# Kernel optimization log

Hardware: AMD Instinct MI355X
Metric: run time of the kernel (lower is better)

The kernel has to match this reference:

```python
import jax, jax.numpy as jnp
import numpy as np

N, E, G = 20000, 320000, 64
DIN, H, EF, FC, OUT = 128, 256, 16, 256, 1
BN_EPS = 1e-5


def _gine_layer(x, src, dst, edge_attr, We, be, Wa, ba, g, bt, Wb, bb):
    # GINEConv (eps=0): out = mlp(x + sum_j relu(x_j + lin_edge(e_ij)))
    e = edge_attr @ We.T + be                      # [E, in_ch]
    m = jax.nn.relu(x[src] + e)                    # messages [E, in_ch]
    agg = jax.ops.segment_sum(m, dst, num_segments=x.shape[0])
    h = (x + agg) @ Wa.T + ba                      # Linear
    # BatchNorm1d in eval mode with running_mean=0, running_var=1
    inv = jax.lax.rsqrt(jnp.asarray(1.0 + BN_EPS, h.dtype))
    h = jax.nn.relu(h * inv * g + bt)
    return jax.nn.relu(h @ Wb.T + bb)


def _mean_pool(h, batch, num_graphs):
    sums = jax.ops.segment_sum(h, batch, num_segments=num_graphs)
    cnt = jax.ops.segment_sum(jnp.ones((h.shape[0],), h.dtype), batch, num_segments=num_graphs)
    return sums / jnp.maximum(cnt, 1.0)[:, None]


def setup_inputs() -> dict:
    key = jax.random.key(0)
    ks = iter(jax.random.split(key, 64))

    def nrm(shape, s=0.05):
        return jax.random.normal(next(ks), shape, jnp.float32) * s

    inp = {
        "x": jax.random.normal(next(ks), (N, DIN), jnp.float32),
        "edge_attr": jax.random.normal(next(ks), (E, EF), jnp.float32),
        "src": jax.random.randint(next(ks), (E,), 0, N),
        "dst": jax.random.randint(next(ks), (E,), 0, N),
        "batch": jnp.sort(jax.random.randint(next(ks), (N,), 0, G)),
    }
    dims = [(DIN, H), (H, H), (H, H)]
    for i, (din, h) in enumerate(dims, start=1):
        inp[f"We{i}"] = nrm((din, EF));  inp[f"be{i}"] = jnp.zeros((din,), jnp.float32)
        inp[f"Wa{i}"] = nrm((h, din));  inp[f"ba{i}"] = jnp.zeros((h,), jnp.float32)
        inp[f"g{i}"] = jnp.ones((h,), jnp.float32); inp[f"bt{i}"] = jnp.zeros((h,), jnp.float32)
        inp[f"Wb{i}"] = nrm((h, h));    inp[f"bb{i}"] = jnp.zeros((h,), jnp.float32)
    inp["L1w"] = nrm((FC * 3, H * 3)); inp["L1b"] = jnp.zeros((FC * 3,), jnp.float32)
    inp["L2w"] = nrm((OUT, FC * 3));   inp["L2b"] = jnp.zeros((OUT,), jnp.float32)
    return inp


def reference(x, edge_attr, src, dst, batch,
              We1, be1, Wa1, ba1, g1, bt1, Wb1, bb1,
              We2, be2, Wa2, ba2, g2, bt2, Wb2, bb2,
              We3, be3, Wa3, ba3, g3, bt3, Wb3, bb3,
              L1w, L1b, L2w, L2b):
    h1 = _gine_layer(x,  src, dst, edge_attr, We1, be1, Wa1, ba1, g1, bt1, Wb1, bb1)
    h2 = _gine_layer(h1, src, dst, edge_attr, We2, be2, Wa2, ba2, g2, bt2, Wb2, bb2)
    h3 = _gine_layer(h2, src, dst, edge_attr, We3, be3, Wa3, ba3, g3, bt3, Wb3, bb3)
    p = jnp.concatenate([_mean_pool(h1, batch, G),
                         _mean_pool(h2, batch, G),
                         _mean_pool(h3, batch, G)], axis=1)   # [G, 3H]
    h = jax.nn.relu(p @ L1w.T + L1b)   # dropout is identity (training=False)
    return jax.nn.sigmoid(h @ L2w.T + L2b)
```

## Files before the change

kernel.cpp:

```cpp
#include <hip/hip_runtime.h>
#include <math.h>
#include <stdint.h>

#define N_NODES 20000
#define M_PAD 20032
#define N_EDGES 320000
#define N_GRAPHS 64
#define DIN 128
#define H 256
#define POOL_W 768
#define CHUNK 40
#define NCHUNK (N_EDGES / CHUNK)

typedef __attribute__((ext_vector_type(8))) short bf16x8;
typedef __attribute__((ext_vector_type(4))) float f32x4;
typedef __attribute__((ext_vector_type(4))) unsigned int u32x4;
typedef __attribute__((ext_vector_type(2))) unsigned int u32x2;
typedef _Float16 h2 __attribute__((ext_vector_type(2)));

__device__ __forceinline__ unsigned short f2bf(float f) {
    unsigned u = __builtin_bit_cast(unsigned, f);
    u += 0x7FFFu + ((u >> 16) & 1u);
    return (unsigned short)(u >> 16);
}
__device__ __forceinline__ float bf2f(unsigned short u) {
    return __builtin_bit_cast(float, (unsigned)u << 16);
}
__device__ __forceinline__ unsigned short f2h(float f) {
    const _Float16 h = (_Float16)f;
    return __builtin_bit_cast(unsigned short, h);
}

#if __has_builtin(__builtin_amdgcn_fdot2)
#define DOT2(a, b, c) __builtin_amdgcn_fdot2((a), (b), (c), false)
#else
__device__ __forceinline__ float dot2_fallback(h2 a, h2 b, float c) {
    return fmaf((float)a.x, (float)b.x, fmaf((float)a.y, (float)b.y, c));
}
#define DOT2(a, b, c) dot2_fallback((a), (b), (c))
#endif

struct CvtJob  { const float* s; unsigned short* d; int n4; int mode; };
struct CvtJobs { CvtJob j[12]; };

__global__ __launch_bounds__(256) void cvt_all(CvtJobs jobs)
{
    const CvtJob J = jobs.j[blockIdx.y];
    if (J.mode == 2) {
        const ushort4 z = {0, 0, 0, 0};
        for (int i = blockIdx.x * 256 + threadIdx.x; i < J.n4; i += gridDim.x * 256)
            ((ushort4*)J.d)[i] = z;
        return;
    }
    if (J.mode == 1) {
        for (int i = blockIdx.x * 256 + threadIdx.x; i < J.n4; i += gridDim.x * 256) {
            const float4 v = ((const float4*)J.s)[i];
            ushort4 r;
            r.x = f2h(v.x); r.y = f2h(v.y); r.z = f2h(v.z); r.w = f2h(v.w);
            ((ushort4*)J.d)[i] = r;
        }
        return;
    }
    for (int i = blockIdx.x * 256 + threadIdx.x; i < J.n4; i += gridDim.x * 256) {
        const float4 v = ((const float4*)J.s)[i];
        ushort4 r;
        r.x = f2bf(v.x); r.y = f2bf(v.y); r.z = f2bf(v.z); r.w = f2bf(v.w);
        ((ushort4*)J.d)[i] = r;
    }
}

__global__ __launch_bounds__(256) void hist_kernel(const int* __restrict__ dst,
                                                   int* __restrict__ deg)
{
    const int i = blockIdx.x * 256 + threadIdx.x;
    if (i < N_EDGES) atomicAdd(deg + dst[i], 1);
}

__global__ __launch_bounds__(1024) void scan_kernel(const int* __restrict__ deg,
                                                    int* __restrict__ off,
                                                    int* __restrict__ cur,
                                                    const int* __restrict__ batch,
                                                    int* __restrict__ start)
{
    __shared__ int wsum[16];
    __shared__ int carry;
    const int tid = threadIdx.x, wave = tid >> 6, lane = tid & 63;
    if (tid == 0) carry = 0;
    __syncthreads();
    for (int base = 0; base < N_NODES; base += 1024) {
        const int i = base + tid;
        const int v = (i < N_NODES) ? deg[i] : 0;
        int s = v;
#pragma unroll
        for (int d = 1; d < 64; d <<= 1) {
            const int t = __shfl_up(s, d);
            if (lane >= d) s += t;
        }
        if (lane == 63) wsum[wave] = s;
        __syncthreads();
        if (wave == 0) {
            int t = (lane < 16) ? wsum[lane] : 0;
#pragma unroll
            for (int d = 1; d < 16; d <<= 1) {
                const int u = __shfl_up(t, d);
                if (lane >= d) t += u;
            }
            if (lane < 16) wsum[lane] = t;
        }
        __syncthreads();
        const int wbase = (wave == 0) ? 0 : wsum[wave - 1];
        if (i < N_NODES) {
            const int o = carry + wbase + s - v;
            off[i] = o;
            cur[i] = o;
        }
        const int tot = wsum[15];
        __syncthreads();
        if (tid == 0) carry += tot;
        __syncthreads();
    }
    if (tid == 0) off[N_NODES] = carry;

    if (tid <= N_GRAPHS) {
        if (tid == N_GRAPHS) { start[N_GRAPHS] = N_NODES; }
        else {
            int lo = 0, hi = N_NODES;
            while (lo < hi) { const int mid = (lo + hi) >> 1; if (batch[mid] < tid) lo = mid + 1; else hi = mid; }
            start[tid] = lo;
        }
    }
}

__global__ __launch_bounds__(256) void chunkmap_kernel(const int* __restrict__ off,
                                                       int* __restrict__ cmap)
{
    const int w = blockIdx.x * 256 + threadIdx.x;
    if (w > NCHUNK) return;
    if (w == NCHUNK) { cmap[w] = N_NODES; return; }
    const int target = w * CHUNK;
    int lo = 0, hi = N_NODES;
    while (lo < hi) { const int mid = (lo + hi) >> 1; if (off[mid] < target) lo = mid + 1; else hi = mid; }
    cmap[w] = lo;
}

__global__ __launch_bounds__(256) void scatter_kernel(
    const int* __restrict__ src, const int* __restrict__ dst,
    const float* __restrict__ ea, int* __restrict__ cursor,
    int* __restrict__ ssrc, unsigned short* __restrict__ eas)
{
    const int e = blockIdx.x * 256 + threadIdx.x;
    if (e < N_EDGES) {
        const int p = atomicAdd(cursor + dst[e], 1);
        ssrc[p] = src[e];
        const float4* er = (const float4*)(ea + (size_t)e * 16);
        unsigned short* dr = eas + (size_t)p * 16;
        ushort4* d4 = (ushort4*)dr;
#pragma unroll
        for (int q = 0; q < 4; ++q) {
            const float4 v = er[q];
            ushort4 r;
            r.x = f2h(v.x); r.y = f2h(v.y); r.z = f2h(v.z); r.w = f2h(v.w);
            d4[q] = r;
        }
    }
}

template<int IN>
__global__ __launch_bounds__(256) void agg3(
    const unsigned short* __restrict__ xb,
    const unsigned short* __restrict__ eas,
    const int* __restrict__ ssrc,
    const int* __restrict__ off,
    const int* __restrict__ cmap,
    const unsigned short* __restrict__ Weh,
    const float* __restrict__ be,
    unsigned short* __restrict__ out)
{
    constexpr int CPL = IN / 64;
    constexpr int XW  = CPL / 2;
    const int lane = threadIdx.x & 63;
    const int wid  = blockIdx.x * 4 + (threadIdx.x >> 6);
    const int c0 = lane * CPL;
    const int zd = __builtin_amdgcn_mbcnt_lo(0u, 0u);

    u32x4 wlo[CPL], whi[CPL];
    float bias[CPL], acc[CPL];
#pragma unroll
    for (int j = 0; j < CPL; ++j) {
        const u32x4* wr = (const u32x4*)(Weh + (size_t)(c0 + j) * 16);
        wlo[j] = wr[0];
        whi[j] = wr[1];
        bias[j] = be[c0 + j];
        acc[j]  = 0.0f;
    }
#pragma unroll
    for (int j = 0; j < CPL; ++j) {
#pragma unroll
        for (int k = 0; k < 4; ++k) {
            { float t = __builtin_bit_cast(float, wlo[j][k]); asm volatile("" : "+v"(t)); wlo[j][k] = __builtin_bit_cast(unsigned int, t); }
            { float t = __builtin_bit_cast(float, whi[j][k]); asm volatile("" : "+v"(t)); whi[j][k] = __builtin_bit_cast(unsigned int, t); }
        }
        asm volatile("" : "+v"(bias[j]));
    }

    int n          = __builtin_amdgcn_readfirstlane(cmap[wid]);
    const int nend = __builtin_amdgcn_readfirstlane(cmap[wid + 1]);
    if (n >= nend) return;
    int p          = __builtin_amdgcn_readfirstlane(off[n]);
    const int pend = __builtin_amdgcn_readfirstlane(off[nend]);

    auto flush = [&](int nn) {
        if constexpr (XW == 2) {
            const u32x2 xs = *(const u32x2*)(xb + (size_t)nn * IN + c0);
            const float x0 = __builtin_bit_cast(float, xs[0] << 16);
            const float x1 = __builtin_bit_cast(float, xs[0] & 0xFFFF0000u);
            const float x2 = __builtin_bit_cast(float, xs[1] << 16);
            const float x3 = __builtin_bit_cast(float, xs[1] & 0xFFFF0000u);
            u32x2 o;
            o[0] = (unsigned)f2bf(x0 + acc[0]) | ((unsigned)f2bf(x1 + acc[1]) << 16);
            o[1] = (unsigned)f2bf(x2 + acc[2]) | ((unsigned)f2bf(x3 + acc[3]) << 16);
            *(u32x2*)(out + (size_t)nn * IN + c0) = o;
        } else {
            const unsigned int xs = *(const unsigned int*)(xb + (size_t)nn * IN + c0);
            const float x0 = __builtin_bit_cast(float, xs << 16);
            const float x1 = __builtin_bit_cast(float, xs & 0xFFFF0000u);
            const unsigned int o =
                (unsigned)f2bf(x0 + acc[0]) | ((unsigned)f2bf(x1 + acc[1]) << 16);
            *(unsigned int*)(out + (size_t)nn * IN + c0) = o;
        }
#pragma unroll
        for (int j = 0; j < CPL; ++j) acc[j] = 0.0f;
    };

    int p1 = __builtin_amdgcn_readfirstlane(off[n + 1]);
    while (p1 == p) {
        flush(n); ++n;
        if (n >= nend) return;
        p1 = __builtin_amdgcn_readfirstlane(off[n + 1]);
    }

    auto ldeL = [&](int q) -> u32x4 {
        return ((const u32x4*)(eas + (size_t)(q + zd) * 16))[0];
    };
    auto ldeH = [&](int q) -> u32x4 {
        return ((const u32x4*)(eas + (size_t)(q + zd) * 16))[1];
    };
    auto ldsrc = [&](int q) -> int {
        const int qc = (q < N_EDGES) ? q : (N_EDGES - 1);
        return ssrc[qc + zd];
    };
    auto ldx = [&](int s) -> u32x2 {
        if constexpr (XW == 2) {
            return *(const u32x2*)(xb + (size_t)s * IN + c0);
        } else {
            u32x2 r;
            r[0] = *(const unsigned int*)(xb + (size_t)s * IN + c0);
            r[1] = 0u;
            return r;
        }
    };
    auto edge_compute = [&](u32x4 eL, u32x4 eH, u32x2 xw) {
        float m[CPL];
#pragma unroll
        for (int j = 0; j < CPL; ++j) m[j] = bias[j];
#pragma unroll
        for (int k = 0; k < 4; ++k) {
            const h2 ep = __builtin_bit_cast(h2, eL[k]);
#pragma unroll
            for (int j = 0; j < CPL; ++j)
                m[j] = DOT2(ep, __builtin_bit_cast(h2, wlo[j][k]), m[j]);
        }
#pragma unroll
        for (int k = 0; k < 4; ++k) {
            const h2 ep = __builtin_bit_cast(h2, eH[k]);
#pragma unroll
            for (int j = 0; j < CPL; ++j)
                m[j] = DOT2(ep, __builtin_bit_cast(h2, whi[j][k]), m[j]);
        }
#pragma unroll
        for (int j = 0; j < CPL; ++j) {
            const unsigned int word = xw[j >> 1];
            const float xf = __builtin_bit_cast(float,
                (j & 1) ? (word & 0xFFFF0000u) : (word << 16));
            acc[j] += fmaxf(m[j] + xf, 0.0f);
        }
    };
    auto adv = [&]() {
        flush(n); ++n;
        while (n < nend) {
            p1 = __builtin_amdgcn_readfirstlane(off[n + 1]);
            if (p1 != p) break;
            flush(n); ++n;
        }
    };

    int sA = ldsrc(p),     sB = ldsrc(p + 1), sC = ldsrc(p + 2), sD = ldsrc(p + 3);
    u32x4 eLA = ldeL(p),     eHA = ldeH(p);
    u32x4 eLB = ldeL(p + 1), eHB = ldeH(p + 1);
    u32x4 eLC = ldeL(p + 2), eHC = ldeH(p + 2);
    u32x4 eLD = ldeL(p + 3), eHD = ldeH(p + 3);
    u32x2 xA = ldx(sA), xB = ldx(sB), xC = ldx(sC), xD = ldx(sD);
    sA = ldsrc(p + 4); sB = ldsrc(p + 5); sC = ldsrc(p + 6); sD = ldsrc(p + 7);

    for (;;) {
        edge_compute(eLA, eHA, xA);
        eLA = ldeL(p + 4); eHA = ldeH(p + 4); xA = ldx(sA); sA = ldsrc(p + 8);
        ++p; if (p == p1) adv();
        if (p >= pend) break;

        edge_compute(eLB, eHB, xB);
        eLB = ldeL(p + 4); eHB = ldeH(p + 4); xB = ldx(sB); sB = ldsrc(p + 8);
        ++p; if (p == p1) adv();
        if (p >= pend) break;

        edge_compute(eLC, eHC, xC);
        eLC = ldeL(p + 4); eHC = ldeH(p + 4); xC = ldx(sC); sC = ldsrc(p + 8);
        ++p; if (p == p1) adv();
        if (p >= pend) break;

        edge_compute(eLD, eHD, xD);
        eLD = ldeL(p + 4); eHD = ldeH(p + 4); xD = ldx(sD); sD = ldsrc(p + 8);
        ++p; if (p == p1) adv();
        if (p >= pend) break;
    }
    while (n < nend) { flush(n); ++n; }
}

template<int K, int EPI>
__global__ __launch_bounds__(256) void gemm_breg2(
    const unsigned short* __restrict__ A,
    const unsigned short* __restrict__ W,
    const float* __restrict__ bias,
    const float* __restrict__ gsc, const float* __restrict__ bsh,
    unsigned short* __restrict__ out)
{
    constexpr int KC = K / 32;
    const int w = threadIdx.x >> 6, lane = threadIdx.x & 63;
    const int lm = lane & 15, lq = lane >> 4;
    const int n0 = (blockIdx.y * 4 + w) * 32;
    const int m0 = blockIdx.x * 64;

    bf16x8 B0[KC], B1[KC];
    {
        const unsigned short* Wp0 = W + (size_t)(n0 + lm) * K + lq * 8;
        const unsigned short* Wp1 = W + (size_t)(n0 + 16 + lm) * K + lq * 8;
#pragma unroll
        for (int c = 0; c < KC; ++c) {
            B0[c] = *(const bf16x8*)(Wp0 + c * 32);
            B1[c] = *(const bf16x8*)(Wp1 + c * 32);
        }
    }

    const float inv = rsqrtf(1.0f + 1e-5f);
    const float bc0 = bias[n0 + lm],      bc1 = bias[n0 + 16 + lm];
    const float gc0 = (EPI == 0) ? gsc[n0 + lm]      : 0.0f;
    const float gc1 = (EPI == 0) ? gsc[n0 + 16 + lm] : 0.0f;
    const float sc0 = (EPI == 0) ? bsh[n0 + lm]      : 0.0f;
    const float sc1 = (EPI == 0) ? bsh[n0 + 16 + lm] : 0.0f;

    bf16x8 aC[KC], aN[KC];
    {
        const unsigned short* Ap = A + (size_t)(m0 + lm) * K + lq * 8;
#pragma unroll
        for (int c = 0; c < KC; ++c) aC[c] = *(const bf16x8*)(Ap + c * 32);
    }

#pragma unroll
    for (int ch = 0; ch < 4; ++ch) {
        if (ch < 3) {
            const unsigned short* Ap = A + (size_t)(m0 + (ch + 1) * 16 + lm) * K + lq * 8;
#pragma unroll
            for (int c = 0; c < KC; ++c) aN[c] = *(const bf16x8*)(Ap + c * 32);
        }

        f32x4 acc0 = (f32x4){0.f, 0.f, 0.f, 0.f};
        f32x4 acc1 = (f32x4){0.f, 0.f, 0.f, 0.f};
#pragma unroll
        for (int c = 0; c < KC; ++c) {
            acc0 = __builtin_amdgcn_mfma_f32_16x16x32_bf16(aC[c], B0[c], acc0, 0, 0, 0);
            acc1 = __builtin_amdgcn_mfma_f32_16x16x32_bf16(aC[c], B1[c], acc1, 0, 0, 0);
        }

        const int mr = m0 + ch * 16;
#pragma unroll
        for (int r = 0; r < 4; ++r) {
            const int row = mr + lq * 4 + r;
            if (EPI == 1 && row >= N_NODES) continue;
            float v0 = acc0[r] + bc0;
            float v1 = acc1[r] + bc1;
            if (EPI == 0) {
                v0 = fmaxf(v0 * inv * gc0 + sc0, 0.0f);
                v1 = fmaxf(v1 * inv * gc1 + sc1, 0.0f);
            } else {
                v0 = fmaxf(v0, 0.0f);
                v1 = fmaxf(v1, 0.0f);
            }
            out[(size_t)row * H + n0 + lm]      = f2bf(v0);
            out[(size_t)row * H + n0 + 16 + lm] = f2bf(v1);
        }

#pragma unroll
        for (int c = 0; c < KC; ++c) aC[c] = aN[c];
    }
}

#define RSPLIT 6
__global__ __launch_bounds__(256) void pool2(
    const unsigned short* __restrict__ h1, const unsigned short* __restrict__ h2,
    const unsigned short* __restrict__ h3, const int* __restrict__ start,
    float* __restrict__ pool)
{
    const int g = blockIdx.x & 63, layer = blockIdx.x >> 6;
    const unsigned short* h = (layer == 0) ? h1 : (layer == 1) ? h2 : h3;
    const int r0 = start[g], r1 = start[g + 1];
    const int nr = r1 - r0;
    if (nr <= 0) return;
    const int chunk = (nr + RSPLIT - 1) / RSPLIT;
    const int rs = r0 + blockIdx.y * chunk;
    const int re = (rs + chunk < r1) ? rs + chunk : r1;
    if (rs >= re) return;

    const int c = threadIdx.x;
    float s0 = 0.f, s1 = 0.f, s2 = 0.f, s3 = 0.f;
    int r = rs;
    for (; r + 4 <= re; r += 4) {
        s0 += bf2f(h[(size_t)(r + 0) * H + c]);
        s1 += bf2f(h[(size_t)(r + 1) * H + c]);
        s2 += bf2f(h[(size_t)(r + 2) * H + c]);
        s3 += bf2f(h[(size_t)(r + 3) * H + c]);
    }
    for (; r < re; ++r) s0 += bf2f(h[(size_t)r * H + c]);
    atomicAdd(&pool[(size_t)g * POOL_W + layer * 256 + c], s0 + s1 + s2 + s3);
}

__global__ __launch_bounds__(256) void fc_head(
    const float* __restrict__ pool, const int* __restrict__ start,
    const float* __restrict__ L1w, const float* __restrict__ L1b,
    const float* __restrict__ L2w, float* __restrict__ gsum)
{
    const int g = blockIdx.x;
    __shared__ float p[POOL_W];

    const float rc = 1.0f / fmaxf((float)(start[g + 1] - start[g]), 1.0f);
    for (int i = threadIdx.x; i < POOL_W; i += 256)
        p[i] = pool[(size_t)g * POOL_W + i] * rc;
    __syncthreads();

    const int wv = threadIdx.x >> 6, lane = threadIdx.x & 63;
    const float4* p4 = (const float4*)p;
    const float4 pa = p4[lane], pb = p4[lane + 64], pc = p4[lane + 128];

    const int ob = blockIdx.y * 64 + wv * 16;
    float part = 0.0f;
#pragma unroll 4
    for (int t = 0; t < 16; ++t) {
        const int o = ob + t;
        const float4* wr = (const float4*)(L1w + (size_t)o * POOL_W);
        const float4 a = wr[lane], b = wr[lane + 64], c = wr[lane + 128];
        float acc = a.x * pa.x + a.y * pa.y + a.z * pa.z + a.w * pa.w
                  + b.x * pb.x + b.y * pb.y + b.z * pb.z + b.w * pb.w
                  + c.x * pc.x + c.y * pc.y + c.z * pc.z + c.w * pc.w;
#pragma unroll
        for (int off = 32; off > 0; off >>= 1) acc += __shfl_xor(acc, off);
        if (lane == 0) part += fmaxf(acc + L1b[o], 0.0f) * L2w[o];
    }
    if (lane == 0) atomicAdd(&gsum[g], part);
}

__global__ __launch_bounds__(64) void sig_kernel(
    const float* __restrict__ gsum, const float* __restrict__ L2b,
    float* __restrict__ out)
{
    const int g = threadIdx.x;
    if (g < N_GRAPHS) out[g] = 1.0f / (1.0f + expf(-(gsum[g] + L2b[0])));
}

extern "C" void kernel_launch(void* const* d_in, const int* in_sizes, int n_in,
                              void* d_out, int out_size, void* d_ws, size_t ws_size,
                              hipStream_t stream)
{
    const float* x     = (const float*)d_in[0];
    const float* ea    = (const float*)d_in[1];
    const int*   src   = (const int*)d_in[2];
    const int*   dst   = (const int*)d_in[3];
    const int*   batch = (const int*)d_in[4];

    const float* We[3]; const float* be[3]; const float* Wa[3]; const float* ba[3];
    const float* gg[3]; const float* bt[3]; const float* Wb[3]; const float* bb[3];
    for (int l = 0; l < 3; ++l) {
        const int o = 5 + 8 * l;
        We[l] = (const float*)d_in[o + 0]; be[l] = (const float*)d_in[o + 1];
        Wa[l] = (const float*)d_in[o + 2]; ba[l] = (const float*)d_in[o + 3];
        gg[l] = (const float*)d_in[o + 4]; bt[l] = (const float*)d_in[o + 5];
        Wb[l] = (const float*)d_in[o + 6]; bb[l] = (const float*)d_in[o + 7];
    }
    const float* L1w = (const float*)d_in[29];
    const float* L1b = (const float*)d_in[30];
    const float* L2w = (const float*)d_in[31];
    const float* L2b = (const float*)d_in[32];

    float* pool   = (float*)d_ws;
    float* gsum   = pool + (size_t)N_GRAPHS * POOL_W;
    int*   deg    = (int*)(gsum + N_GRAPHS);
    int*   off    = deg + N_NODES;
    int*   cursor = off + N_NODES + 1;
    int*   start  = cursor + N_NODES;
    int*   cmap   = start + 72;
    int*   ssrc   = (int*)((((uintptr_t)(cmap + NCHUNK + 1)) + 31) & ~(uintptr_t)31);
    unsigned short* eas = (unsigned short*)((((uintptr_t)(ssrc + N_EDGES + 16)) + 31) & ~(uintptr_t)31);
    unsigned short* xb = (unsigned short*)((((uintptr_t)(eas + (size_t)(N_EDGES + 16) * 16)) + 31) & ~(uintptr_t)31);
    unsigned short* u  = xb + (size_t)M_PAD * DIN;
    unsigned short* tT = u  + (size_t)M_PAD * H;
    unsigned short* h1 = tT + (size_t)M_PAD * H;
    unsigned short* h2 = h1 + (size_t)M_PAD * H;
    unsigned short* h3 = h2 + (size_t)M_PAD * H;
    unsigned short* wbf[6];
    wbf[0] = h3 + (size_t)M_PAD * H;
    wbf[1] = wbf[0] + H * DIN;
    for (int i = 2; i < 6; ++i) wbf[i] = wbf[i - 1] + H * H;
    unsigned short* weh[3];
    weh[0] = wbf[5] + H * H;
    weh[1] = weh[0] + DIN * 16;
    weh[2] = weh[1] + H * 16;

    CvtJobs jobs;
    jobs.j[0]  = { x,       xb,                    N_NODES * DIN / 4,       0 };
    jobs.j[1]  = { Wa[0],   wbf[0],                H * DIN / 4,             0 };
    jobs.j[2]  = { Wb[0],   wbf[1],                H * H / 4,               0 };
    jobs.j[3]  = { Wa[1],   wbf[2],                H * H / 4,               0 };
    jobs.j[4]  = { Wb[1],   wbf[3],                H * H / 4,               0 };
    jobs.j[5]  = { Wa[2],   wbf[4],                H * H / 4,               0 };
    jobs.j[6]  = { Wb[2],   wbf[5],                H * H / 4,               0 };
    jobs.j[7]  = { nullptr, (unsigned short*)deg,  N_NODES * 4 / 8,         2 };
    jobs.j[8]  = { nullptr, (unsigned short*)pool, (N_GRAPHS * POOL_W + N_GRAPHS) * 4 / 8, 2 };
    jobs.j[9]  = { We[0],   weh[0],                DIN * 16 / 4,            1 };
    jobs.j[10] = { We[1],   weh[1],                H * 16 / 4,              1 };
    jobs.j[11] = { We[2],   weh[2],                H * 16 / 4,              1 };
    cvt_all<<<dim3(320, 12), 256, 0, stream>>>(jobs);

    hist_kernel<<<(N_EDGES + 255) / 256, 256, 0, stream>>>(dst, deg);
    scan_kernel<<<1, 1024, 0, stream>>>(deg, off, cursor, batch, start);
    chunkmap_kernel<<<(NCHUNK + 256) / 256, 256, 0, stream>>>(off, cmap);
    scatter_kernel<<<(N_EDGES + 255) / 256, 256, 0, stream>>>(src, dst, ea, cursor, ssrc, eas);

    const int  agrid = NCHUNK / 4;
    const dim3 ggrid(M_PAD / 64, 2);

    agg3<DIN><<<agrid, 256, 0, stream>>>(xb, eas, ssrc, off, cmap, weh[0], be[0], u);
    gemm_breg2<DIN, 0><<<ggrid, 256, 0, stream>>>(u, wbf[0], ba[0], gg[0], bt[0], tT);
    gemm_breg2<H,   1><<<ggrid, 256, 0, stream>>>(tT, wbf[1], bb[0], nullptr, nullptr, h1);
    agg3<H><<<agrid, 256, 0, stream>>>(h1, eas, ssrc, off, cmap, weh[1], be[1], u);
    gemm_breg2<H, 0><<<ggrid, 256, 0, stream>>>(u, wbf[2], ba[1], gg[1], bt[1], tT);
    gemm_breg2<H, 1><<<ggrid, 256, 0, stream>>>(tT, wbf[3], bb[1], nullptr, nullptr, h2);
    agg3<H><<<agrid, 256, 0, stream>>>(h2, eas, ssrc, off, cmap, weh[2], be[2], u);
    gemm_breg2<H, 0><<<ggrid, 256, 0, stream>>>(u, wbf[4], ba[2], gg[2], bt[2], tT);
    gemm_breg2<H, 1><<<ggrid, 256, 0, stream>>>(tT, wbf[5], bb[2], nullptr, nullptr, h3);

    pool2<<<dim3(3 * N_GRAPHS, RSPLIT), 256, 0, stream>>>(h1, h2, h3, start, pool);
    fc_head<<<dim3(N_GRAPHS, POOL_W / 64), 256, 0, stream>>>(pool, start, L1w, L1b, L2w, gsum);
    sig_kernel<<<1, 64, 0, stream>>>(gsum, L2b, (float*)d_out);
}
```

Baseline: 521.9 us.

## Stage GEMM A tile in swizzled LDS and prefetch self-node features in aggregation

```diff
diff --git a/kernel.cpp b/kernel.cpp
--- a/kernel.cpp
+++ b/kernel.cpp
@@ -209,9 +209,18 @@
     int p          = __builtin_amdgcn_readfirstlane(off[n]);
     const int pend = __builtin_amdgcn_readfirstlane(off[nend]);
 
-    auto flush = [&](int nn) {
+    auto ldx = [&](int s) -> u32x2 {
         if constexpr (XW == 2) {
-            const u32x2 xs = *(const u32x2*)(xb + (size_t)nn * IN + c0);
+            return *(const u32x2*)(xb + (size_t)s * IN + c0);
+        } else {
+            u32x2 r;
+            r[0] = *(const unsigned int*)(xb + (size_t)s * IN + c0);
+            r[1] = 0u;
+            return r;
+        }
+    };
+    auto flushv = [&](int nn, u32x2 xs) {
+        if constexpr (XW == 2) {
             const float x0 = __builtin_bit_cast(float, xs[0] << 16);
             const float x1 = __builtin_bit_cast(float, xs[0] & 0xFFFF0000u);
             const float x2 = __builtin_bit_cast(float, xs[1] << 16);
@@ -221,9 +230,8 @@
             o[1] = (unsigned)f2bf(x2 + acc[2]) | ((unsigned)f2bf(x3 + acc[3]) << 16);
             *(u32x2*)(out + (size_t)nn * IN + c0) = o;
         } else {
-            const unsigned int xs = *(const unsigned int*)(xb + (size_t)nn * IN + c0);
-            const float x0 = __builtin_bit_cast(float, xs << 16);
-            const float x1 = __builtin_bit_cast(float, xs & 0xFFFF0000u);
+            const float x0 = __builtin_bit_cast(float, xs[0] << 16);
+            const float x1 = __builtin_bit_cast(float, xs[0] & 0xFFFF0000u);
             const unsigned int o =
                 (unsigned)f2bf(x0 + acc[0]) | ((unsigned)f2bf(x1 + acc[1]) << 16);
             *(unsigned int*)(out + (size_t)nn * IN + c0) = o;
@@ -234,10 +242,11 @@
 
     int p1 = __builtin_amdgcn_readfirstlane(off[n + 1]);
     while (p1 == p) {
-        flush(n); ++n;
+        flushv(n, ldx(n)); ++n;
         if (n >= nend) return;
         p1 = __builtin_amdgcn_readfirstlane(off[n + 1]);
     }
+    u32x2 xself = ldx(n);
 
     auto ldeL = [&](int q) -> u32x4 {
         return ((const u32x4*)(eas + (size_t)(q + zd) * 16))[0];
@@ -248,16 +257,6 @@
     auto ldsrc = [&](int q) -> int {
         const int qc = (q < N_EDGES) ? q : (N_EDGES - 1);
         return ssrc[qc + zd];
-    };
-    auto ldx = [&](int s) -> u32x2 {
-        if constexpr (XW == 2) {
-            return *(const u32x2*)(xb + (size_t)s * IN + c0);
-        } else {
-            u32x2 r;
-            r[0] = *(const unsigned int*)(xb + (size_t)s * IN + c0);
-            r[1] = 0u;
-            return r;
-        }
     };
     auto edge_compute = [&](u32x4 eL, u32x4 eH, u32x2 xw) {
         float m[CPL];
@@ -286,11 +285,11 @@
         }
     };
     auto adv = [&]() {
-        flush(n); ++n;
+        flushv(n, xself); ++n;
         while (n < nend) {
             p1 = __builtin_amdgcn_readfirstlane(off[n + 1]);
-            if (p1 != p) break;
-            flush(n); ++n;
+            if (p1 != p) { xself = ldx(n); break; }
+            flushv(n, ldx(n)); ++n;
         }
     };
 
@@ -323,11 +322,11 @@
         ++p; if (p == p1) adv();
         if (p >= pend) break;
     }
-    while (n < nend) { flush(n); ++n; }
+    while (n < nend) { flushv(n, ldx(n)); ++n; }
 }
 
 template<int K, int EPI>
-__global__ __launch_bounds__(256) void gemm_breg2(
+__global__ __launch_bounds__(256) void gemm_ldsA(
     const unsigned short* __restrict__ A,
     const unsigned short* __restrict__ W,
     const float* __restrict__ bias,
@@ -335,10 +334,21 @@
     unsigned short* __restrict__ out)
 {
     constexpr int KC = K / 32;
+    constexpr int SLOTS = K / 8;
+    __shared__ unsigned short Al[64 * K];
+
     const int w = threadIdx.x >> 6, lane = threadIdx.x & 63;
     const int lm = lane & 15, lq = lane >> 4;
     const int n0 = (blockIdx.y * 4 + w) * 32;
     const int m0 = blockIdx.x * 64;
+
+#pragma unroll
+    for (int i = 0; i < 64 * SLOTS / 256; ++i) {
+        const int t = i * 256 + threadIdx.x;
+        const int row = t / SLOTS, slot = t % SLOTS;
+        const uint4 v = *(const uint4*)(A + (size_t)(m0 + row) * K + slot * 8);
+        *(uint4*)((char*)Al + row * (K * 2) + ((slot ^ (row & 7)) * 16)) = v;
+    }
 
     bf16x8 B0[KC], B1[KC];
     {
@@ -358,19 +368,17 @@
     const float sc0 = (EPI == 0) ? bsh[n0 + lm]      : 0.0f;
     const float sc1 = (EPI == 0) ? bsh[n0 + 16 + lm] : 0.0f;
 
-    bf16x8 aC[KC], aN[KC];
-    {
-        const unsigned short* Ap = A + (size_t)(m0 + lm) * K + lq * 8;
-#pragma unroll
-        for (int c = 0; c < KC; ++c) aC[c] = *(const bf16x8*)(Ap + c * 32);
-    }
+    __syncthreads();
 
 #pragma unroll
     for (int ch = 0; ch < 4; ++ch) {
-        if (ch < 3) {
-            const unsigned short* Ap = A + (size_t)(m0 + (ch + 1) * 16 + lm) * K + lq * 8;
-#pragma unroll
-            for (int c = 0; c < KC; ++c) aN[c] = *(const bf16x8*)(Ap + c * 32);
+        const int row = ch * 16 + lm;
+        const char* rbase = (const char*)Al + row * (K * 2);
+        bf16x8 aC[KC];
+#pragma unroll
+        for (int c = 0; c < KC; ++c) {
+            const int slot = (lq + c * 4) ^ (row & 7);
+            aC[c] = *(const bf16x8*)(rbase + slot * 16);
         }
 
         f32x4 acc0 = (f32x4){0.f, 0.f, 0.f, 0.f};
@@ -384,8 +392,8 @@
         const int mr = m0 + ch * 16;
 #pragma unroll
         for (int r = 0; r < 4; ++r) {
-            const int row = mr + lq * 4 + r;
-            if (EPI == 1 && row >= N_NODES) continue;
+            const int rowo = mr + lq * 4 + r;
+            if (EPI == 1 && rowo >= N_NODES) continue;
             float v0 = acc0[r] + bc0;
             float v1 = acc1[r] + bc1;
             if (EPI == 0) {
@@ -395,12 +403,9 @@
                 v0 = fmaxf(v0, 0.0f);
                 v1 = fmaxf(v1, 0.0f);
             }
-            out[(size_t)row * H + n0 + lm]      = f2bf(v0);
-            out[(size_t)row * H + n0 + 16 + lm] = f2bf(v1);
-        }
-
-#pragma unroll
-        for (int c = 0; c < KC; ++c) aC[c] = aN[c];
+            out[(size_t)rowo * H + n0 + lm]      = f2bf(v0);
+            out[(size_t)rowo * H + n0 + 16 + lm] = f2bf(v1);
+        }
     }
 }
 
@@ -547,14 +552,14 @@
     const dim3 ggrid(M_PAD / 64, 2);
 
     agg3<DIN><<<agrid, 256, 0, stream>>>(xb, eas, ssrc, off, cmap, weh[0], be[0], u);
-    gemm_breg2<DIN, 0><<<ggrid, 256, 0, stream>>>(u, wbf[0], ba[0], gg[0], bt[0], tT);
-    gemm_breg2<H,   1><<<ggrid, 256, 0, stream>>>(tT, wbf[1], bb[0], nullptr, nullptr, h1);
+    gemm_ldsA<DIN, 0><<<ggrid, 256, 0, stream>>>(u, wbf[0], ba[0], gg[0], bt[0], tT);
+    gemm_ldsA<H,   1><<<ggrid, 256, 0, stream>>>(tT, wbf[1], bb[0], nullptr, nullptr, h1);
     agg3<H><<<agrid, 256, 0, stream>>>(h1, eas, ssrc, off, cmap, weh[1], be[1], u);
-    gemm_breg2<H, 0><<<ggrid, 256, 0, stream>>>(u, wbf[2], ba[1], gg[1], bt[1], tT);
-    gemm_breg2<H, 1><<<ggrid, 256, 0, stream>>>(tT, wbf[3], bb[1], nullptr, nullptr, h2);
+    gemm_ldsA<H, 0><<<ggrid, 256, 0, stream>>>(u, wbf[2], ba[1], gg[1], bt[1], tT);
+    gemm_ldsA<H, 1><<<ggrid, 256, 0, stream>>>(tT, wbf[3], bb[1], nullptr, nullptr, h2);
     agg3<H><<<agrid, 256, 0, stream>>>(h2, eas, ssrc, off, cmap, weh[2], be[2], u);
-    gemm_breg2<H, 0><<<ggrid, 256, 0, stream>>>(u, wbf[4], ba[2], gg[2], bt[2], tT);
-    gemm_breg2<H, 1><<<ggrid, 256, 0, stream>>>(tT, wbf[5], bb[2], nullptr, nullptr, h3);
+    gemm_ldsA<H, 0><<<ggrid, 256, 0, stream>>>(u, wbf[4], ba[2], gg[2], bt[2], tT);
+    gemm_ldsA<H, 1><<<ggrid, 256, 0, stream>>>(tT, wbf[5], bb[2], nullptr, nullptr, h3);
 
     pool2<<<dim3(3 * N_GRAPHS, RSPLIT), 256, 0, stream>>>(h1, h2, h3, start, pool);
     fc_head<<<dim3(N_GRAPHS, POOL_W / 64), 256, 0, stream>>>(pool, start, L1w, L1b, L2w, gsum);
```

New measurement: 481.2 us. -7.8%, faster.
